# Kernel tuning notes

Hardware: AMD Instinct MI355X
Metric: run time of the kernel (lower is better)

The kernel has to match this reference:

```python
import jax, jax.numpy as jnp
import numpy as np

DIM, H, D, B, L = 1024, 8, 64, 1, 256


def silu(v):
    return v * jax.nn.sigmoid(v)


def setup_inputs() -> dict:
    key = jax.random.key(0)
    ks = jax.random.split(key, 12)
    n = lambda i, shape, scale=1.0: jax.random.normal(ks[i], shape, dtype=jnp.float32) * scale
    return {
        "x": n(0, (B, L, DIM)),
        "hidden_real": n(1, (B, H, D)),
        "hidden_imag": n(2, (B, H, D)),
        "w_in1": n(3, (DIM, DIM), 1.0 / np.sqrt(DIM)),
        "b_in1": jnp.zeros((DIM,), jnp.float32),
        "w_in2": n(4, (DIM, H * D * 4), 1.0 / np.sqrt(DIM)),
        "b_in2": jnp.zeros((H * D * 4,), jnp.float32),
        "w_out1": n(5, (H * D * 2, DIM), 1.0 / np.sqrt(H * D * 2)),
        "b_out1": jnp.zeros((DIM,), jnp.float32),
        "w_out2": n(6, (DIM, DIM), 1.0 / np.sqrt(DIM)),
        "b_out2": jnp.zeros((DIM,), jnp.float32),
        "mat_v_real": n(7, (H, D, D)),
        "mat_v_imag": n(8, (H, D, D)),
    }


def reference(x, hidden_real, hidden_imag, w_in1, b_in1, w_in2, b_in2,
              w_out1, b_out1, w_out2, b_out2, mat_v_real, mat_v_imag):
    batch, slen, _ = x.shape
    t = silu(x @ w_in1 + b_in1)
    t = t @ w_in2 + b_in2                       # (B, L, 4*H*D)
    z = t.reshape(batch, slen, H, D, 2, 2)      # [..., {x,a}, {re,im}]
    xc = jax.lax.complex(z[..., 0, 0], z[..., 0, 1])   # (B, L, H, D) complex
    ac = jax.lax.complex(z[..., 1, 0], z[..., 1, 1])

    # normalize a: unit phase * sigmoid(log(|a|^2)) magnitude
    mag2 = ac.real * ac.real + ac.imag * ac.imag
    ac = ac * (jax.lax.rsqrt(mag2) * jax.nn.sigmoid(jnp.log(mag2)))

    a_ln = jnp.log(ac)                          # (B, L, H, D) complex
    al = jnp.transpose(a_ln, (0, 2, 3, 1))      # (B, H, D, L)

    # triu-broadcast + cumsum along cols == the FFT conv-with-ones in the original
    idx = jnp.arange(slen)
    triu = idx[:, None] <= idx[None, :]          # row i, col j: keep j >= i
    tri = jnp.where(triu, al[..., None, :], 0.0)  # (B, H, D, L, L)
    cum = jnp.cumsum(tri, axis=-1)               # cum[i, k] = sum_{j=i..k} a_ln[j]
    keep = (idx[:, None] - 1) <= idx[None, :]    # triu(diagonal=-1)
    c = jnp.where(keep, jnp.exp(cum), 0.0)       # c[i,k] = prod_{j=i..k} a[j]; c[i,i-1]=1

    V = jax.lax.complex(mat_v_real, mat_v_imag)  # (H, D, D)
    Vinv = jnp.linalg.inv(V)
    hidden = jax.lax.complex(hidden_real, hidden_imag)  # (B, H, D)

    x_roll = jnp.concatenate([hidden.astype(xc.dtype)[:, None], xc[:, :-1]], axis=1)
    u = jnp.einsum('hno,blho->blhn', Vinv, x_roll)       # V^{-1} applied per head
    h = jnp.einsum('bholm,blho->bmho', c, u)             # banded product-scan
    h = h.at[:, -1].add(jnp.einsum('hno,bho->bhn', Vinv, xc[:, -1]))
    h = jnp.einsum('hno,blho->blhn', V, h)               # back to V-basis

    hidden_next = h[:, -1]                                # (B, H, D) complex
    hr = jnp.stack([h.real, h.imag], axis=-1).reshape(batch, slen, H * D * 2)
    y = silu(hr @ w_out1 + b_out1)
    y = y @ w_out2 + b_out2
    return y, hidden_next
```

## Files before the change

### kernel.cpp

```cpp
#include <hip/hip_runtime.h>
#include <math.h>

#define DIMN 1024
#define NH 8
#define ND 64
#define LSEQ 256
#define HD 512

typedef __attribute__((ext_vector_type(8))) short short8;
typedef __attribute__((ext_vector_type(4))) float f32x4;

__device__ __forceinline__ float2 cmul(float2 a, float2 b){
    return make_float2(a.x*b.x - a.y*b.y, a.x*b.y + a.y*b.x);
}
__device__ __forceinline__ ushort f2bf(float f){
    union { float f; unsigned u; } v; v.f = f;
    unsigned r = v.u + 0x7FFF + ((v.u >> 16) & 1);
    return (ushort)(r >> 16);
}

#define ISTR 65
#define ASTR 40
#define BK 32

__device__ __forceinline__ void inv_gj_blocked(const float* __restrict__ Vr,
        const float* __restrict__ Vi, float2* __restrict__ Vinv,
        int h, int tid, float2* Mx){
    for (int idx = tid; idx < 4096; idx += 512){
        int i = idx >> 6, j = idx & 63;
        Mx[i*ISTR + j] = make_float2(Vr[h*4096 + idx], Vi[h*4096 + idx]);
    }
    __syncthreads();
    const int w = tid >> 6, l = tid & 63;
    const int rbase = w*8;
    for (int kb = 0; kb < 8; ++kb){
        const int k0 = kb*8;
        if (w == 0){
            float2 pr[8];
            #pragma unroll
            for (int m = 0; m < 8; ++m) pr[m] = Mx[l*ISTR + k0 + m];
            #pragma unroll
            for (int k = 0; k < 8; ++k){
                const int gk = k0 + k;
                float2 d; d.x = __shfl(pr[k].x, gk); d.y = __shfl(pr[k].y, gk);
                float im = 1.f/(d.x*d.x + d.y*d.y);
                float2 p = make_float2(d.x*im, -d.y*im);
                float2 spr[8];
                #pragma unroll
                for (int m = 0; m < 8; ++m){
                    float2 t; t.x = __shfl(pr[m].x, gk); t.y = __shfl(pr[m].y, gk);
                    spr[m] = (m == k) ? p : cmul(t, p);
                }
                float2 f = pr[k];
                if (l == gk){
                    #pragma unroll
                    for (int m = 0; m < 8; ++m) pr[m] = spr[m];
                } else {
                    #pragma unroll
                    for (int m = 0; m < 8; ++m){
                        float2 u = cmul(f, spr[m]);
                        if (m == k){ pr[m].x = -u.x;  pr[m].y = -u.y;  }
                        else       { pr[m].x -= u.x;  pr[m].y -= u.y;  }
                    }
                }
            }
            #pragma unroll
            for (int m = 0; m < 8; ++m) Mx[l*ISTR + k0 + m] = pr[m];
        }
        __syncthreads();
        float2 br[8];
        #pragma unroll
        for (int m = 0; m < 8; ++m) br[m] = Mx[(k0+m)*ISTR + l];
        __syncthreads();
        if (((unsigned)(l - k0)) >= 8u){
            #pragma unroll
            for (int rr = 0; rr < 8; ++rr){
                const int r = rbase + rr;
                float2 acc;
                if (((unsigned)(r - k0)) < 8u){ acc.x = 0.f; acc.y = 0.f; }
                else acc = Mx[r*ISTR + l];
                #pragma unroll
                for (int m = 0; m < 8; ++m){
                    float2 Pv = Mx[r*ISTR + k0 + m];
                    acc.x += Pv.x*br[m].x - Pv.y*br[m].y;
                    acc.y += Pv.x*br[m].y + Pv.y*br[m].x;
                }
                Mx[r*ISTR + l] = acc;
            }
        }
        __syncthreads();
    }
    for (int idx = tid; idx < 4096; idx += 512){
        int i = idx >> 6, j = idx & 63;
        Vinv[h*4096 + idx] = Mx[i*ISTR + j];
    }
}

__device__ __forceinline__ void w3eff_tile(const float* __restrict__ Vr,
        const float* __restrict__ Vi, const float* __restrict__ w3,
        ushort* __restrict__ W3bt, int t, int tid, float* lds){
    const int n0 = (t & 31)*32;
    const int c0 = (t >> 5)*32;
    const int h  = c0 >> 7;
    const int og0 = (c0 & 127) >> 1;
    float* Vbr = lds;
    float* Vbi = lds + 1024;
    float* Wb  = lds + 2048;
    for (int q = tid; q < 1024; q += 512){
        int dd = q >> 4, oo = q & 15;
        Vbr[q] = Vr[(h*64+dd)*64 + og0 + oo];
        Vbi[q] = Vi[(h*64+dd)*64 + og0 + oo];
    }
    for (int q = tid; q < 4096; q += 512){
        int row = q >> 5, nn = q & 31;
        Wb[q] = w3[(h*128 + row)*1024 + n0 + nn];
    }
    __syncthreads();
    const int nn = tid & 31, oo = tid >> 5;
    float ar = 0.f, ai = 0.f;
    #pragma unroll 8
    for (int dd = 0; dd < 64; ++dd){
        float vr = Vbr[dd*16 + oo], vi = Vbi[dd*16 + oo];
        float w0 = Wb[(dd*2)*32 + nn], w1v = Wb[(dd*2+1)*32 + nn];
        ar += vr*w0 + vi*w1v;
        ai += -vi*w0 + vr*w1v;
    }
    W3bt[(n0+nn)*1024 + c0 + oo*2 + 0] = f2bf(ar);
    W3bt[(n0+nn)*1024 + c0 + oo*2 + 1] = f2bf(ai);
}

__global__ __launch_bounds__(512) void prep_kernel(
        const float* __restrict__ x,
        const float* __restrict__ w1, const float* __restrict__ w2,
        const float* __restrict__ w3, const float* __restrict__ w4,
        const float* __restrict__ Vr, const float* __restrict__ Vi,
        ushort* __restrict__ x_bf,
        ushort* __restrict__ w1t, ushort* __restrict__ w2t,
        ushort* __restrict__ w4t, ushort* __restrict__ W3bt,
        float2* __restrict__ Vinv){
    __shared__ __align__(16) char lds_raw[33280];
    const int b = blockIdx.x;
    const int tid = threadIdx.x;
    const int half = tid >> 8;

    if (b < 8){
        inv_gj_blocked(Vr, Vi, Vinv, b, tid, (float2*)lds_raw);
        return;
    }
    int u = b - 8;
    if (u < 2048){
        const float* W; ushort* Wt; const int K = 1024; int N; int t;
        if (u < 512)      { W = w1; Wt = w1t; N = 1024; t = u*2 + half; }
        else if (u < 1536){ W = w2; Wt = w2t; N = 2048; t = (u-512)*2 + half; }
        else              { W = w4; Wt = w4t; N = 1024; t = (u-1536)*2 + half; }
        const int tiles_n = N >> 5;
        const int n0 = (t % tiles_n) * 32, k0 = (t / tiles_n) * 32;
        float* tile = (float*)lds_raw + half*(32*33);
        const int tx = tid & 31, ty = (tid >> 5) & 7;
        #pragma unroll
        for (int i = 0; i < 4; ++i)
            tile[(ty + i*8)*33 + tx] = W[(k0 + ty + i*8)*N + n0 + tx];
        __syncthreads();
        #pragma unroll
        for (int i = 0; i < 4; ++i){
            int r = ty + i*8;
            Wt[(n0 + r)*K + k0 + tx] = f2bf(tile[tx*33 + r]);
        }
        return;
    }
    u -= 2048;
    if (u < 64){
        const int base = (u*512 + tid)*2;
        #pragma unroll
        for (int j = 0; j < 2; ++j){
            float4 v = ((const float4*)x)[base + j];
            ushort4 uu; uu.x=f2bf(v.x); uu.y=f2bf(v.y); uu.z=f2bf(v.z); uu.w=f2bf(v.w);
            ((ushort4*)x_bf)[base + j] = uu;
        }
        return;
    }
    u -= 64;
    w3eff_tile(Vr, Vi, w3, W3bt, u, tid, (float*)lds_raw);
}

template<int ACT, int KS>
__device__ __forceinline__ void gemm_phase(const ushort* __restrict__ A,
        const ushort* __restrict__ Bt, const float* __restrict__ bias,
        float* __restrict__ Cf, ushort* __restrict__ Cb,
        float2* __restrict__ XCo, float2* __restrict__ Ao,
        int M, int N, int blk, int tid, float* red){
    constexpr int Kw = 1024/KS;
    constexpr int TPBT = 8/KS;
    const int wave = tid >> 6, l = tid & 63;
    const int ml = l & 15, quad = l >> 4;
    const int lt = wave / KS, ks = wave - lt*KS;
    const int tile = blk*TPBT + lt;
    const int tm = M >> 5;
    const int bm = (tile % tm)*32, bn = (tile / tm)*32;
    const ushort* Ap = A  + (bm + ml)*1024 + ks*Kw + quad*8;
    const ushort* Bp = Bt + (bn + ml)*1024 + ks*Kw + quad*8;

    f32x4 acc[2][2];
    #pragma unroll
    for (int i=0;i<2;++i)
        #pragma unroll
        for (int j=0;j<2;++j) acc[i][j] = (f32x4){0.f,0.f,0.f,0.f};

    short8 ac[2], bc[2];
    ac[0] = *(const short8*)(Ap);
    ac[1] = *(const short8*)(Ap + 16*1024);
    bc[0] = *(const short8*)(Bp);
    bc[1] = *(const short8*)(Bp + 16*1024);

    #pragma unroll
    for (int k0 = 32; k0 < Kw; k0 += 32){
        short8 an[2], bn2[2];
        an[0]  = *(const short8*)(Ap + k0);
        an[1]  = *(const short8*)(Ap + 16*1024 + k0);
        bn2[0] = *(const short8*)(Bp + k0);
        bn2[1] = *(const short8*)(Bp + 16*1024 + k0);
        #pragma unroll
        for (int i=0;i<2;++i)
            #pragma unroll
            for (int j=0;j<2;++j)
                acc[i][j] = __builtin_amdgcn_mfma_f32_16x16x32_bf16(ac[i], bc[j], acc[i][j], 0,0,0);
        ac[0]=an[0]; ac[1]=an[1]; bc[0]=bn2[0]; bc[1]=bn2[1];
    }
    #pragma unroll
    for (int i=0;i<2;++i)
        #pragma unroll
        for (int j=0;j<2;++j)
            acc[i][j] = __builtin_amdgcn_mfma_f32_16x16x32_bf16(ac[i], bc[j], acc[i][j], 0,0,0);

    #pragma unroll
    for (int i=0;i<2;++i)
        #pragma unroll
        for (int j=0;j<2;++j)
            #pragma unroll
            for (int r=0;r<4;++r)
                red[wave*1024 + ((i*2+j)*4+r)*64 + l] = acc[i][j][r];
    __syncthreads();

    if (ks == 0){
        #pragma unroll
        for (int i=0;i<2;++i){
            #pragma unroll
            for (int j=0;j<2;++j){
                const int gcol = bn + j*16 + ml;
                const float bsv = bias[gcol];
                #pragma unroll
                for (int r=0;r<4;++r){
                    float val = bsv;
                    #pragma unroll
                    for (int s=0;s<KS;++s)
                        val += red[(wave+s)*1024 + ((i*2+j)*4+r)*64 + l];
                    const int grow = bm + i*16 + quad*4 + r;
                    if (ACT == 2){
                        float v1 = __shfl_down(val, 1);
                        float v2 = __shfl_down(val, 2);
                        float v3 = __shfl_down(val, 3);
                        if ((l & 3) == 0){
                            int hd = gcol >> 2;
                            XCo[grow*HD + hd] = make_float2(val, v1);
                            float m2 = v2*v2 + v3*v3;
                            float s = sqrtf(m2)/(1.f + m2);
                            Ao[grow*HD + hd] = make_float2(v2*s, v3*s);
                        }
                    } else if (ACT == 1){
                        val *= 1.f/(1.f + expf(-val));
                        Cb[grow*N + gcol] = f2bf(val);
                    } else {
                        Cf[grow*N + gcol] = val;
                    }
                }
            }
        }
    }
}

template<int ACT, int KS>
__global__ __launch_bounds__(512) void gemm_ks(const ushort* __restrict__ A,
        const ushort* __restrict__ Bt, const float* __restrict__ bias,
        float* __restrict__ Cf, ushort* __restrict__ Cb,
        float2* __restrict__ XCo, float2* __restrict__ Ao,
        int M, int N,
        const float* __restrict__ tVr, const float* __restrict__ tVi,
        const float2* __restrict__ S255, float* __restrict__ out_tail,
        int tail_n){
    __shared__ float red[8*1024];
    const int nt = (M >> 5) * (N >> 5);
    const int ntb = nt / (8/KS);
    if (out_tail != nullptr && blockIdx.x >= ntb){
        if ((threadIdx.x >> 6) == 0 && tail_n >= 512){
            const int l = threadIdx.x & 63;
            for (int hn = l; hn < 512; hn += 64){
                const int h = hn >> 6;
                float2 acc2 = make_float2(0.f, 0.f);
                #pragma unroll 8
                for (int o = 0; o < 64; ++o){
                    float2 v = make_float2(tVr[hn*64+o], tVi[hn*64+o]);
                    float2 p = cmul(v, S255[h*64+o]);
                    acc2.x += p.x; acc2.y += p.y;
                }
                if (tail_n >= 1024){
                    out_tail[hn]       = acc2.x;
                    out_tail[512 + hn] = acc2.y;
                } else {
                    out_tail[hn] = acc2.x;
                }
            }
        }
        return;
    }
    gemm_phase<ACT, KS>(A, Bt, bias, Cf, Cb, XCo, Ao, M, N,
                        blockIdx.x, threadIdx.x, red);
}

__global__ __launch_bounds__(512) void inv_kernel(const float* __restrict__ Vr,
                                                  const float* __restrict__ Vi,
                                                  float2* __restrict__ Vinv){
    __shared__ float2 Mx[64*ISTR];
    inv_gj_blocked(Vr, Vi, Vinv, blockIdx.x, threadIdx.x, Mx);
}

__global__ __launch_bounds__(256) void transpose_cvt(const float* __restrict__ W,
                 ushort* __restrict__ Wt, int K, int N){
    __shared__ float tile[32][33];
    const int n0 = blockIdx.x * 32, k0 = blockIdx.y * 32;
    const int tx = threadIdx.x & 31, ty = threadIdx.x >> 5;
    #pragma unroll
    for (int i = 0; i < 4; ++i)
        tile[ty + i*8][tx] = W[(k0 + ty + i*8)*N + n0 + tx];
    __syncthreads();
    #pragma unroll
    for (int i = 0; i < 4; ++i){
        int r = ty + i*8;
        Wt[(n0 + r)*K + k0 + tx] = f2bf(tile[tx][r]);
    }
}

__global__ __launch_bounds__(256) void cvt_bf16_kernel(const float* __restrict__ in,
                                 ushort* __restrict__ o, int n4){
    int i = blockIdx.x*256 + threadIdx.x;
    if (i < n4){
        float4 v = ((const float4*)in)[i];
        ushort4 u; u.x=f2bf(v.x); u.y=f2bf(v.y); u.z=f2bf(v.z); u.w=f2bf(v.w);
        ((ushort4*)o)[i] = u;
    }
}

#define BM 64
#define BN 64
template<int ACT>
__global__ __launch_bounds__(256) void gemm_bt(const ushort* __restrict__ A,
                 const ushort* __restrict__ Bt, const float* __restrict__ bias,
                 float* __restrict__ Cf, ushort* __restrict__ Cb,
                 float2* __restrict__ XCo, float2* __restrict__ Ao,
                 int M, int N, int K,
                 const float* __restrict__ tVr, const float* __restrict__ tVi,
                 const float2* __restrict__ S255, float* __restrict__ out_tail,
                 int tail_n){
    __shared__ ushort As[BM*ASTR];
    __shared__ ushort Bs[BN*ASTR];
    const int tid = threadIdx.x;
    const int bm = blockIdx.y * BM, bn = blockIdx.x * BN;
    const int wave = tid >> 6, l = tid & 63;
    const int wr = (wave >> 1) * 32, wc = (wave & 1) * 32;
    const int ml = l & 15, quad = l >> 4;

    if (ACT == 0 && out_tail != nullptr && blockIdx.x == 0 && blockIdx.y == 0){
        for (int hn = tid; hn < 512; hn += 256){
            int h = hn >> 6;
            float2 acc2 = make_float2(0.f, 0.f);
            #pragma unroll 8
            for (int o = 0; o < 64; ++o){
                float2 v = make_float2(tVr[hn*64+o], tVi[hn*64+o]);
                float2 p = cmul(v, S255[h*64+o]);
                acc2.x += p.x; acc2.y += p.y;
            }
            if (tail_n >= 1024){
                out_tail[hn]       = acc2.x;
                out_tail[512 + hn] = acc2.y;
            } else if (tail_n >= 512){
                out_tail[hn] = acc2.x;
            }
        }
    }

    f32x4 acc[2][2];
    #pragma unroll
    for (int i=0;i<2;++i)
        #pragma unroll
        for (int j=0;j<2;++j) acc[i][j] = (f32x4){0.f,0.f,0.f,0.f};
    const int c0r = tid >> 2;
    const int c0s = tid & 3;
    for (int k0 = 0; k0 < K; k0 += BK){
        uint4 av = *(const uint4*)&A [(bm + c0r)*K + k0 + c0s*8];
        uint4 bv = *(const uint4*)&Bt[(bn + c0r)*K + k0 + c0s*8];
        __syncthreads();
        *(uint4*)&As[c0r*ASTR + c0s*8] = av;
        *(uint4*)&Bs[c0r*ASTR + c0s*8] = bv;
        __syncthreads();
        short8 af[2], bfv[2];
        #pragma unroll
        for (int f=0; f<2; ++f){
            af[f]  = *(const short8*)&As[(wr + f*16 + ml)*ASTR + quad*8];
            bfv[f] = *(const short8*)&Bs[(wc + f*16 + ml)*ASTR + quad*8];
        }
        #pragma unroll
        for (int i=0;i<2;++i)
            #pragma unroll
            for (int j=0;j<2;++j)
                acc[i][j] = __builtin_amdgcn_mfma_f32_16x16x32_bf16(af[i], bfv[j], acc[i][j], 0,0,0);
    }
    #pragma unroll
    for (int i=0;i<2;++i){
        #pragma unroll
        for (int j=0;j<2;++j){
            const int gcol = bn + wc + j*16 + ml;
            const float bsv = bias[gcol];
            #pragma unroll
            for (int r=0;r<4;++r){
                const int grow = bm + wr + i*16 + quad*4 + r;
                float val = acc[i][j][r] + bsv;
                if (ACT == 2){
                    float v1 = __shfl_down(val, 1);
                    float v2 = __shfl_down(val, 2);
                    float v3 = __shfl_down(val, 3);
                    if ((l & 3) == 0){
                        int hd = gcol >> 2;
                        XCo[grow*HD + hd] = make_float2(val, v1);
                        float m2 = v2*v2 + v3*v3;
                        float s = sqrtf(m2)/(1.f + m2);
                        Ao[grow*HD + hd] = make_float2(v2*s, v3*s);
                    }
                } else if (ACT == 1){
                    val *= 1.f/(1.f + expf(-val));
                    Cb[grow*N + gcol] = f2bf(val);
                } else {
                    Cf[grow*N + gcol] = val;
                }
            }
        }
    }
}

__global__ __launch_bounds__(512) void upscan_kernel(const float2* __restrict__ Vinv,
        const float* __restrict__ hidr, const float* __restrict__ him,
        const float2* __restrict__ XC, const float2* __restrict__ Aseq,
        ushort* __restrict__ Sb, float2* __restrict__ S255){
    __shared__ float4 buf[2][2][LSEQ];
    __shared__ float2 vrow[2][64];
    __shared__ float2 inu[2];
    const int b = blockIdx.x;
    const int tid = threadIdx.x;
    const int g = tid >> 8, m = tid & 255;
    const int hn = b*2 + g;
    const int h = hn >> 6;
    if (m < 64) vrow[g][m] = Vinv[hn*64 + m];
    __syncthreads();
    float2 acc = make_float2(0.f, 0.f);
    const float2* xrow = &XC[m*HD + h*64];
    #pragma unroll 8
    for (int o=0;o<64;++o){
        float2 p = cmul(vrow[g][o], xrow[o]);
        acc.x += p.x; acc.y += p.y;
    }
    if (m == 0){
        float2 i0 = make_float2(0.f, 0.f);
        #pragma unroll 8
        for (int o=0;o<64;++o){
            float2 hv = make_float2(hidr[h*64+o], him[h*64+o]);
            float2 p = cmul(vrow[g][o], hv);
            i0.x += p.x; i0.y += p.y;
        }
        inu[g] = i0;
    }
    float2 a = Aseq[m*HD + hn];
    buf[0][g][m] = make_float4(a.x, a.y, acc.x, acc.y);
    __syncthreads();
    int pb = 0;
    #pragma unroll
    for (int d = 1; d < LSEQ; d <<= 1){
        float4 cur = buf[pb][g][m];
        float4 o2 = cur;
        if (m >= d){
            float4 prev = buf[pb][g][m-d];
            float2 cA = make_float2(cur.x, cur.y), cU = make_float2(cur.z, cur.w);
            float2 pA = make_float2(prev.x, prev.y), pU = make_float2(prev.z, prev.w);
            float2 nA = cmul(cA, pA);
            float2 nU = cmul(cA, pU);
            nU.x += cU.x; nU.y += cU.y;
            o2 = make_float4(nA.x, nA.y, nU.x, nU.y);
        }
        buf[pb^1][g][m] = o2;
        pb ^= 1;
        __syncthreads();
    }
    float4 t = buf[pb][g][m];
    float2 init = inu[g];
    float2 st = cmul(make_float2(t.x, t.y), init);
    st.x += t.z; st.y += t.w;
    Sb[m*DIMN + hn*2]   = f2bf(st.x);
    Sb[m*DIMN + hn*2+1] = f2bf(st.y);
    if (m == LSEQ-1) S255[hn] = st;
}

__global__ __launch_bounds__(256) void vmul_kernel(const float* __restrict__ Vr,
                            const float* __restrict__ Vi,
                            const float2* __restrict__ S, ushort* __restrict__ hrb,
                            float* __restrict__ out_tail, int tail_n){
    int g = blockIdx.x*256 + threadIdx.x;
    int m = g >> 9, hn = g & 511;
    int h = hn >> 6;
    const float* vr = &Vr[hn*64];
    const float* vi = &Vi[hn*64];
    const float2* srow = &S[m*HD + h*64];
    float2 acc = make_float2(0.f, 0.f);
    #pragma unroll 8
    for (int o=0;o<64;++o){
        float2 v = make_float2(vr[o], vi[o]);
        float2 p = cmul(v, srow[o]);
        acc.x += p.x; acc.y += p.y;
    }
    hrb[m*DIMN + hn*2]   = f2bf(acc.x);
    hrb[m*DIMN + hn*2+1] = f2bf(acc.y);
    if (m == LSEQ-1){
        if (tail_n >= 1024){
            out_tail[hn]       = acc.x;
            out_tail[512 + hn] = acc.y;
        } else if (tail_n >= 512){
            out_tail[hn] = acc.x;
        }
    }
}

__global__ __launch_bounds__(512) void upscan_f32_kernel(const float2* __restrict__ Vinv,
        const float* __restrict__ hidr, const float* __restrict__ him,
        const float2* __restrict__ XC, const float2* __restrict__ Aseq,
        float2* __restrict__ S){
    __shared__ float4 buf[2][2][LSEQ];
    __shared__ float2 vrow[2][64];
    __shared__ float2 inu[2];
    const int b = blockIdx.x;
    const int tid = threadIdx.x;
    const int g = tid >> 8, m = tid & 255;
    const int hn = b*2 + g;
    const int h = hn >> 6;
    if (m < 64) vrow[g][m] = Vinv[hn*64 + m];
    __syncthreads();
    float2 acc = make_float2(0.f, 0.f);
    const float2* xrow = &XC[m*HD + h*64];
    #pragma unroll 8
    for (int o=0;o<64;++o){
        float2 p = cmul(vrow[g][o], xrow[o]);
        acc.x += p.x; acc.y += p.y;
    }
    if (m == 0){
        float2 i0 = make_float2(0.f, 0.f);
        #pragma unroll 8
        for (int o=0;o<64;++o){
            float2 hv = make_float2(hidr[h*64+o], him[h*64+o]);
            float2 p = cmul(vrow[g][o], hv);
            i0.x += p.x; i0.y += p.y;
        }
        inu[g] = i0;
    }
    float2 a = Aseq[m*HD + hn];
    buf[0][g][m] = make_float4(a.x, a.y, acc.x, acc.y);
    __syncthreads();
    int pb = 0;
    #pragma unroll
    for (int d = 1; d < LSEQ; d <<= 1){
        float4 cur = buf[pb][g][m];
        float4 o2 = cur;
        if (m >= d){
            float4 prev = buf[pb][g][m-d];
            float2 cA = make_float2(cur.x, cur.y), cU = make_float2(cur.z, cur.w);
            float2 pA = make_float2(prev.x, prev.y), pU = make_float2(prev.z, prev.w);
            float2 nA = cmul(cA, pA);
            float2 nU = cmul(cA, pU);
            nU.x += cU.x; nU.y += cU.y;
            o2 = make_float4(nA.x, nA.y, nU.x, nU.y);
        }
        buf[pb^1][g][m] = o2;
        pb ^= 1;
        __syncthreads();
    }
    float4 t = buf[pb][g][m];
    float2 init = inu[g];
    float2 st = cmul(make_float2(t.x, t.y), init);
    st.x += t.z; st.y += t.w;
    S[m*HD + hn] = st;
}

extern "C" void kernel_launch(void* const* d_in, const int* in_sizes, int n_in,
                              void* d_out, int out_size, void* d_ws, size_t ws_size,
                              hipStream_t stream) {
    const float* x      = (const float*)d_in[0];
    const float* hidr   = (const float*)d_in[1];
    const float* hidi   = (const float*)d_in[2];
    const float* w_in1  = (const float*)d_in[3];
    const float* b_in1  = (const float*)d_in[4];
    const float* w_in2  = (const float*)d_in[5];
    const float* b_in2  = (const float*)d_in[6];
    const float* w_out1 = (const float*)d_in[7];
    const float* b_out1 = (const float*)d_in[8];
    const float* w_out2 = (const float*)d_in[9];
    const float* b_out2 = (const float*)d_in[10];
    const float* Vr     = (const float*)d_in[11];
    const float* Vi     = (const float*)d_in[12];
    float* out = (float*)d_out;
    const int tail_n = out_size - LSEQ*DIMN;
    char* ws = (char*)d_ws;

    if (ws_size >= 14946304u){
        float2* Vinv  = (float2*)(ws + 0);
        ushort* w2t   = (ushort*)(ws + 262144);
        ushort* W3bt  = (ushort*)(ws + 4456448);
        ushort* w4t   = (ushort*)(ws + 6553600);
        ushort* w1t   = (ushort*)(ws + 8650752);
        float2* XC    = (float2*)(ws + 8650752);
        float2* Aseq  = (float2*)(ws + 9699328);
        ushort* x_bf  = (ushort*)(ws + 10747904);
        float2* S255  = (float2*)(ws + 10747904);
        ushort* t1_bf = (ushort*)(ws + 11272192);
        ushort* y1_bf = (ushort*)(ws + 11796480);
        ushort* Sb    = t1_bf;

        prep_kernel<<<3144, 512, 0, stream>>>(x, w_in1, w_in2, w_out1, w_out2,
                                              Vr, Vi, x_bf, w1t, w2t, w4t, W3bt, Vinv);
        gemm_ks<1,8><<<256, 512, 0, stream>>>(x_bf, w1t, b_in1, nullptr, t1_bf,
                nullptr, nullptr, LSEQ, DIMN, nullptr, nullptr, nullptr, nullptr, 0);
        gemm_ks<2,4><<<256, 512, 0, stream>>>(t1_bf, w2t, b_in2, nullptr, nullptr,
                XC, Aseq, LSEQ, 2048, nullptr, nullptr, nullptr, nullptr, 0);
        upscan_kernel<<<256, 512, 0, stream>>>(Vinv, hidr, hidi, XC, Aseq, Sb, S255);
        gemm_ks<1,8><<<257, 512, 0, stream>>>(Sb, W3bt, b_out1, nullptr, y1_bf,
                nullptr, nullptr, LSEQ, DIMN, Vr, Vi, S255, out + LSEQ*DIMN, tail_n);
        gemm_ks<0,8><<<256, 512, 0, stream>>>(y1_bf, w4t, b_out2, out, nullptr,
                nullptr, nullptr, LSEQ, DIMN, nullptr, nullptr, nullptr, nullptr, 0);
    } else {
        float2* Vinv  = (float2*)(ws + 0);
        ushort* wt    = (ushort*)(ws + 262144);
        ushort* x_bf  = (ushort*)(ws + 4456448);
        ushort* t1_bf = (ushort*)(ws + 4980736);
        float2* XC    = (float2*)(ws + 5505024);
        float2* Aseq  = (float2*)(ws + 6553600);
        float2* S     = (float2*)(ws + 7602176);
        ushort* y1_bf = x_bf;
        ushort* hr_bf = t1_bf;

        inv_kernel<<<NH, 512, 0, stream>>>(Vr, Vi, Vinv);
        cvt_bf16_kernel<<<LSEQ*DIMN/4/256, 256, 0, stream>>>(x, x_bf, LSEQ*DIMN/4);
        transpose_cvt<<<dim3(32,32), 256, 0, stream>>>(w_in1, wt, DIMN, DIMN);
        gemm_bt<1><<<dim3(16,4), 256, 0, stream>>>(x_bf, wt, b_in1, nullptr, t1_bf,
                nullptr, nullptr, LSEQ, DIMN, DIMN, nullptr, nullptr, nullptr, nullptr, 0);
        transpose_cvt<<<dim3(64,32), 256, 0, stream>>>(w_in2, wt, DIMN, 2048);
        gemm_bt<2><<<dim3(32,4), 256, 0, stream>>>(t1_bf, wt, b_in2, nullptr, nullptr,
                XC, Aseq, LSEQ, 2048, DIMN, nullptr, nullptr, nullptr, nullptr, 0);
        upscan_f32_kernel<<<256, 512, 0, stream>>>(Vinv, hidr, hidi, XC, Aseq, S);
        vmul_kernel<<<LSEQ*HD/256, 256, 0, stream>>>(Vr, Vi, S, hr_bf, out + LSEQ*DIMN, tail_n);
        transpose_cvt<<<dim3(32,32), 256, 0, stream>>>(w_out1, wt, DIMN, DIMN);
        gemm_bt<1><<<dim3(16,4), 256, 0, stream>>>(hr_bf, wt, b_out1, nullptr, y1_bf,
                nullptr, nullptr, LSEQ, DIMN, DIMN, nullptr, nullptr, nullptr, nullptr, 0);
        transpose_cvt<<<dim3(32,32), 256, 0, stream>>>(w_out2, wt, DIMN, DIMN);
        gemm_bt<0><<<dim3(16,4), 256, 0, stream>>>(y1_bf, wt, b_out2, out, nullptr,
                nullptr, nullptr, LSEQ, DIMN, DIMN, nullptr, nullptr, nullptr, nullptr, 0);
    }
}
```

Before: 193.9 us.

## Move W3 and W4 weight prep into the first two GEMM launches as extra blocks

The W3-effective tile construction and the w4 transpose/bf16 conversion are taken out of the prep kernel. They now run as extra blocks appended to the first and second GEMM launches, so this weight preparation overlaps with GEMM work instead of lengthening the serial prep stage. The cost is larger grids for those GEMMs. The extra blocks also share the machine with the GEMM tiles and may delay them. Shared memory in the GEMM kernel is resized to fit the transpose buffers.

```diff
diff --git a/kernel.cpp b/kernel.cpp
--- a/kernel.cpp
+++ b/kernel.cpp
@@ -132,11 +132,9 @@
 __global__ __launch_bounds__(512) void prep_kernel(
         const float* __restrict__ x,
         const float* __restrict__ w1, const float* __restrict__ w2,
-        const float* __restrict__ w3, const float* __restrict__ w4,
         const float* __restrict__ Vr, const float* __restrict__ Vi,
         ushort* __restrict__ x_bf,
         ushort* __restrict__ w1t, ushort* __restrict__ w2t,
-        ushort* __restrict__ w4t, ushort* __restrict__ W3bt,
         float2* __restrict__ Vinv){
     __shared__ __align__(16) char lds_raw[33280];
     const int b = blockIdx.x;
@@ -148,11 +146,10 @@
         return;
     }
     int u = b - 8;
-    if (u < 2048){
+    if (u < 1536){
         const float* W; ushort* Wt; const int K = 1024; int N; int t;
-        if (u < 512)      { W = w1; Wt = w1t; N = 1024; t = u*2 + half; }
-        else if (u < 1536){ W = w2; Wt = w2t; N = 2048; t = (u-512)*2 + half; }
-        else              { W = w4; Wt = w4t; N = 1024; t = (u-1536)*2 + half; }
+        if (u < 512){ W = w1; Wt = w1t; N = 1024; t = u*2 + half; }
+        else        { W = w2; Wt = w2t; N = 2048; t = (u-512)*2 + half; }
         const int tiles_n = N >> 5;
         const int n0 = (t % tiles_n) * 32, k0 = (t / tiles_n) * 32;
         float* tile = (float*)lds_raw + half*(32*33);
@@ -168,19 +165,14 @@
         }
         return;
     }
-    u -= 2048;
-    if (u < 64){
-        const int base = (u*512 + tid)*2;
-        #pragma unroll
-        for (int j = 0; j < 2; ++j){
-            float4 v = ((const float4*)x)[base + j];
-            ushort4 uu; uu.x=f2bf(v.x); uu.y=f2bf(v.y); uu.z=f2bf(v.z); uu.w=f2bf(v.w);
-            ((ushort4*)x_bf)[base + j] = uu;
-        }
-        return;
-    }
-    u -= 64;
-    w3eff_tile(Vr, Vi, w3, W3bt, u, tid, (float*)lds_raw);
+    u -= 1536;
+    const int base = (u*512 + tid)*2;
+    #pragma unroll
+    for (int j = 0; j < 2; ++j){
+        float4 v = ((const float4*)x)[base + j];
+        ushort4 uu; uu.x=f2bf(v.x); uu.y=f2bf(v.y); uu.z=f2bf(v.z); uu.w=f2bf(v.w);
+        ((ushort4*)x_bf)[base + j] = uu;
+    }
 }
 
 template<int ACT, int KS>
@@ -276,6 +268,45 @@
             }
         }
     }
+}
+
+template<int ACT, int KS, int RIDE>
+__global__ __launch_bounds__(512) void gemm_ride(const ushort* __restrict__ A,
+        const ushort* __restrict__ Bt, const float* __restrict__ bias,
+        float* __restrict__ Cf, ushort* __restrict__ Cb,
+        float2* __restrict__ XCo, float2* __restrict__ Ao,
+        int M, int N,
+        const float* __restrict__ Vr, const float* __restrict__ Vi,
+        const float* __restrict__ w3, ushort* __restrict__ W3bt,
+        const float* __restrict__ w4, ushort* __restrict__ w4t){
+    __shared__ __align__(16) char lds_raw[33280];
+    const int nt = (M >> 5) * (N >> 5);
+    const int ntb = nt / (8/KS);
+    if ((int)blockIdx.x >= ntb){
+        const int u = (int)blockIdx.x - ntb;
+        const int tid = threadIdx.x;
+        if (RIDE == 1){
+            w3eff_tile(Vr, Vi, w3, W3bt, u, tid, (float*)lds_raw);
+        } else {
+            const int half = tid >> 8;
+            const int t = u*2 + half;
+            const int n0 = (t & 31)*32, k0 = (t >> 5)*32;
+            float* tile = (float*)lds_raw + half*(32*33);
+            const int tx = tid & 31, ty = (tid >> 5) & 7;
+            #pragma unroll
+            for (int i = 0; i < 4; ++i)
+                tile[(ty + i*8)*33 + tx] = w4[(k0 + ty + i*8)*1024 + n0 + tx];
+            __syncthreads();
+            #pragma unroll
+            for (int i = 0; i < 4; ++i){
+                int r = ty + i*8;
+                w4t[(n0 + r)*1024 + k0 + tx] = f2bf(tile[tx*33 + r]);
+            }
+        }
+        return;
+    }
+    gemm_phase<ACT, KS>(A, Bt, bias, Cf, Cb, XCo, Ao, M, N,
+                        blockIdx.x, threadIdx.x, (float*)lds_raw);
 }
 
 template<int ACT, int KS>
@@ -628,12 +659,12 @@
         ushort* y1_bf = (ushort*)(ws + 11796480);
         ushort* Sb    = t1_bf;
 
-        prep_kernel<<<3144, 512, 0, stream>>>(x, w_in1, w_in2, w_out1, w_out2,
-                                              Vr, Vi, x_bf, w1t, w2t, w4t, W3bt, Vinv);
-        gemm_ks<1,8><<<256, 512, 0, stream>>>(x_bf, w1t, b_in1, nullptr, t1_bf,
-                nullptr, nullptr, LSEQ, DIMN, nullptr, nullptr, nullptr, nullptr, 0);
-        gemm_ks<2,4><<<256, 512, 0, stream>>>(t1_bf, w2t, b_in2, nullptr, nullptr,
-                XC, Aseq, LSEQ, 2048, nullptr, nullptr, nullptr, nullptr, 0);
+        prep_kernel<<<1608, 512, 0, stream>>>(x, w_in1, w_in2, Vr, Vi,
+                                              x_bf, w1t, w2t, Vinv);
+        gemm_ride<1,8,1><<<1280, 512, 0, stream>>>(x_bf, w1t, b_in1, nullptr, t1_bf,
+                nullptr, nullptr, LSEQ, DIMN, Vr, Vi, w_out1, W3bt, nullptr, nullptr);
+        gemm_ride<2,4,2><<<768, 512, 0, stream>>>(t1_bf, w2t, b_in2, nullptr, nullptr,
+                XC, Aseq, LSEQ, 2048, nullptr, nullptr, nullptr, nullptr, w_out2, w4t);
         upscan_kernel<<<256, 512, 0, stream>>>(Vinv, hidr, hidi, XC, Aseq, Sb, S255);
         gemm_ks<1,8><<<257, 512, 0, stream>>>(Sb, W3bt, b_out1, nullptr, y1_bf,
                 nullptr, nullptr, LSEQ, DIMN, Vr, Vi, S255, out + LSEQ*DIMN, tail_n);
```

After: 202.0 us. 1.04x slower.

## Fuse first GEMM into prep kernel reading fp32 inputs directly

Applied to the files above, without the earlier changes.

Drops the separate x-to-bf16 conversion and w_in1 transpose-to-bf16 passes. The first GEMM (x@w_in1 + bias, silu) now runs as 64x64 MFMA tiles inside the prep kernel, converting fp32 operands to bf16 in LDS on the fly, and is merged with the weight preparation for the later layers. This removes one kernel launch and the round trip of w1t and x_bf through memory. Blocks doing the matrix inversion get raised wave priority so that work, which sits on the critical path, keeps pace while sharing the GPU with the transpose blocks. The cost is that the first GEMM now uses only 32 blocks with strided scalar B loads, so it exposes less parallelism than before.

```diff
diff --git a/kernel.cpp b/kernel.cpp
--- a/kernel.cpp
+++ b/kernel.cpp
@@ -26,6 +26,7 @@
 __device__ __forceinline__ void inv_gj_blocked(const float* __restrict__ Vr,
         const float* __restrict__ Vi, float2* __restrict__ Vinv,
         int h, int tid, float2* Mx){
+    __builtin_amdgcn_s_setprio(1);
     for (int idx = tid; idx < 4096; idx += 512){
         int i = idx >> 6, j = idx & 63;
         Mx[i*ISTR + j] = make_float2(Vr[h*4096 + idx], Vi[h*4096 + idx]);
@@ -90,6 +91,7 @@
         }
         __syncthreads();
     }
+    __builtin_amdgcn_s_setprio(0);
     for (int idx = tid; idx < 4096; idx += 512){
         int i = idx >> 6, j = idx & 63;
         Vinv[h*4096 + idx] = Mx[i*ISTR + j];
@@ -129,58 +131,112 @@
     W3bt[(n0+nn)*1024 + c0 + oo*2 + 1] = f2bf(ai);
 }
 
-__global__ __launch_bounds__(512) void prep_kernel(
+__device__ __forceinline__ void gemm1_direct_tile(const float* __restrict__ x,
+        const float* __restrict__ w1, const float* __restrict__ bias,
+        ushort* __restrict__ Cb, int tile, int tid8, ushort* lds){
+    ushort* As = lds;
+    ushort* Bs = lds + 64*ASTR;
+    const int bm = (tile & 3)*64, bn = (tile >> 2)*64;
+    const int wave = tid8 >> 6, l = tid8 & 63;
+    const int wr = (wave >> 1)*32, wc = (wave & 1)*32;
+    const int ml = l & 15, quad = l >> 4;
+    f32x4 acc[2][2];
+    #pragma unroll
+    for (int i=0;i<2;++i)
+        #pragma unroll
+        for (int j=0;j<2;++j) acc[i][j] = (f32x4){0.f,0.f,0.f,0.f};
+    const int c0r = tid8 >> 2, c0s = tid8 & 3;
+    const int bn_n = tid8 & 63, bk0 = (tid8 >> 6)*8;
+    for (int k0 = 0; k0 < DIMN; k0 += BK){
+        float4 a0 = *(const float4*)&x[(bm+c0r)*DIMN + k0 + c0s*8];
+        float4 a1 = *(const float4*)&x[(bm+c0r)*DIMN + k0 + c0s*8 + 4];
+        float bv[8];
+        #pragma unroll
+        for (int kk = 0; kk < 8; ++kk)
+            bv[kk] = w1[(k0 + bk0 + kk)*DIMN + bn + bn_n];
+        __syncthreads();
+        ushort4 u0; u0.x=f2bf(a0.x); u0.y=f2bf(a0.y); u0.z=f2bf(a0.z); u0.w=f2bf(a0.w);
+        ushort4 u1; u1.x=f2bf(a1.x); u1.y=f2bf(a1.y); u1.z=f2bf(a1.z); u1.w=f2bf(a1.w);
+        *(ushort4*)&As[c0r*ASTR + c0s*8]     = u0;
+        *(ushort4*)&As[c0r*ASTR + c0s*8 + 4] = u1;
+        #pragma unroll
+        for (int kk = 0; kk < 8; ++kk)
+            Bs[bn_n*ASTR + bk0 + kk] = f2bf(bv[kk]);
+        __syncthreads();
+        short8 af[2], bfv[2];
+        #pragma unroll
+        for (int f=0; f<2; ++f){
+            af[f]  = *(const short8*)&As[(wr + f*16 + ml)*ASTR + quad*8];
+            bfv[f] = *(const short8*)&Bs[(wc + f*16 + ml)*ASTR + quad*8];
+        }
+        #pragma unroll
+        for (int i=0;i<2;++i)
+            #pragma unroll
+            for (int j=0;j<2;++j)
+                acc[i][j] = __builtin_amdgcn_mfma_f32_16x16x32_bf16(af[i], bfv[j], acc[i][j], 0,0,0);
+    }
+    #pragma unroll
+    for (int i=0;i<2;++i){
+        #pragma unroll
+        for (int j=0;j<2;++j){
+            const int gcol = bn + wc + j*16 + ml;
+            const float bsv = bias[gcol];
+            #pragma unroll
+            for (int r=0;r<4;++r){
+                const int grow = bm + wr + i*16 + quad*4 + r;
+                float val = acc[i][j][r] + bsv;
+                val *= 1.f/(1.f + expf(-val));
+                Cb[grow*DIMN + gcol] = f2bf(val);
+            }
+        }
+    }
+}
+
+__global__ __launch_bounds__(512) void mix1_kernel(
         const float* __restrict__ x,
         const float* __restrict__ w1, const float* __restrict__ w2,
         const float* __restrict__ w3, const float* __restrict__ w4,
         const float* __restrict__ Vr, const float* __restrict__ Vi,
-        ushort* __restrict__ x_bf,
-        ushort* __restrict__ w1t, ushort* __restrict__ w2t,
-        ushort* __restrict__ w4t, ushort* __restrict__ W3bt,
-        float2* __restrict__ Vinv){
+        const float* __restrict__ b1,
+        ushort* __restrict__ t1_bf,
+        ushort* __restrict__ w2t, ushort* __restrict__ W3bt,
+        ushort* __restrict__ w4t, float2* __restrict__ Vinv){
     __shared__ __align__(16) char lds_raw[33280];
     const int b = blockIdx.x;
     const int tid = threadIdx.x;
     const int half = tid >> 8;
 
-    if (b < 8){
-        inv_gj_blocked(Vr, Vi, Vinv, b, tid, (float2*)lds_raw);
+    if (b < 32){
+        gemm1_direct_tile(x, w1, b1, t1_bf, b*2 + half, tid & 255,
+                          (ushort*)lds_raw + half*(128*ASTR));
         return;
     }
-    int u = b - 8;
-    if (u < 2048){
-        const float* W; ushort* Wt; const int K = 1024; int N; int t;
-        if (u < 512)      { W = w1; Wt = w1t; N = 1024; t = u*2 + half; }
-        else if (u < 1536){ W = w2; Wt = w2t; N = 2048; t = (u-512)*2 + half; }
-        else              { W = w4; Wt = w4t; N = 1024; t = (u-1536)*2 + half; }
-        const int tiles_n = N >> 5;
-        const int n0 = (t % tiles_n) * 32, k0 = (t / tiles_n) * 32;
-        float* tile = (float*)lds_raw + half*(32*33);
-        const int tx = tid & 31, ty = (tid >> 5) & 7;
-        #pragma unroll
-        for (int i = 0; i < 4; ++i)
-            tile[(ty + i*8)*33 + tx] = W[(k0 + ty + i*8)*N + n0 + tx];
-        __syncthreads();
-        #pragma unroll
-        for (int i = 0; i < 4; ++i){
-            int r = ty + i*8;
-            Wt[(n0 + r)*K + k0 + tx] = f2bf(tile[tx*33 + r]);
-        }
+    if (b < 40){
+        inv_gj_blocked(Vr, Vi, Vinv, b - 32, tid, (float2*)lds_raw);
         return;
     }
-    u -= 2048;
-    if (u < 64){
-        const int base = (u*512 + tid)*2;
-        #pragma unroll
-        for (int j = 0; j < 2; ++j){
-            float4 v = ((const float4*)x)[base + j];
-            ushort4 uu; uu.x=f2bf(v.x); uu.y=f2bf(v.y); uu.z=f2bf(v.z); uu.w=f2bf(v.w);
-            ((ushort4*)x_bf)[base + j] = uu;
-        }
+    int widx = b - 40;
+    if (widx >= 1536){
+        w3eff_tile(Vr, Vi, w3, W3bt, widx - 1536, tid, (float*)lds_raw);
         return;
     }
-    u -= 64;
-    w3eff_tile(Vr, Vi, w3, W3bt, u, tid, (float*)lds_raw);
+    const float* W; ushort* Wt; int K = 1024, N;
+    if (widx < 1024){ W = w2; Wt = w2t; N = 2048; }
+    else            { W = w4; Wt = w4t; N = 1024; widx -= 1024; }
+    const int t = widx*2 + half;
+    const int tiles_n = N >> 5;
+    const int n0 = (t % tiles_n) * 32, k0 = (t / tiles_n) * 32;
+    float* tile = (float*)lds_raw + half*(32*33);
+    const int tx = tid & 31, ty = (tid >> 5) & 7;
+    #pragma unroll
+    for (int i = 0; i < 4; ++i)
+        tile[(ty + i*8)*33 + tx] = W[(k0 + ty + i*8)*N + n0 + tx];
+    __syncthreads();
+    #pragma unroll
+    for (int i = 0; i < 4; ++i){
+        int r = ty + i*8;
+        Wt[(n0 + r)*K + k0 + tx] = f2bf(tile[tx*33 + r]);
+    }
 }
 
 template<int ACT, int KS>
@@ -619,19 +675,15 @@
         ushort* w2t   = (ushort*)(ws + 262144);
         ushort* W3bt  = (ushort*)(ws + 4456448);
         ushort* w4t   = (ushort*)(ws + 6553600);
-        ushort* w1t   = (ushort*)(ws + 8650752);
         float2* XC    = (float2*)(ws + 8650752);
         float2* Aseq  = (float2*)(ws + 9699328);
-        ushort* x_bf  = (ushort*)(ws + 10747904);
         float2* S255  = (float2*)(ws + 10747904);
         ushort* t1_bf = (ushort*)(ws + 11272192);
         ushort* y1_bf = (ushort*)(ws + 11796480);
         ushort* Sb    = t1_bf;
 
-        prep_kernel<<<3144, 512, 0, stream>>>(x, w_in1, w_in2, w_out1, w_out2,
-                                              Vr, Vi, x_bf, w1t, w2t, w4t, W3bt, Vinv);
-        gemm_ks<1,8><<<256, 512, 0, stream>>>(x_bf, w1t, b_in1, nullptr, t1_bf,
-                nullptr, nullptr, LSEQ, DIMN, nullptr, nullptr, nullptr, nullptr, 0);
+        mix1_kernel<<<2600, 512, 0, stream>>>(x, w_in1, w_in2, w_out1, w_out2,
+                                              Vr, Vi, b_in1, t1_bf, w2t, W3bt, w4t, Vinv);
         gemm_ks<2,4><<<256, 512, 0, stream>>>(t1_bf, w2t, b_in2, nullptr, nullptr,
                 XC, Aseq, LSEQ, 2048, nullptr, nullptr, nullptr, nullptr, 0);
         upscan_kernel<<<256, 512, 0, stream>>>(Vinv, hidr, hidi, XC, Aseq, Sb, S255);
```

After: 185.4 us. 4.4% less time.
